# Kernel optimization log

Hardware: AMD Instinct MI355X
Metric: run time of the kernel (lower is better)

Reference implementation:

```python
import jax, jax.numpy as jnp
import numpy as np

N = 50000
E = 400000
F_IN = 128
NUM_CLASSES = 16
# (heads, out_channels, concat) per GATConv layer
LAYERS = [(8, 32, True), (8, 16, True), (8, 8, True), (1, NUM_CLASSES, False)]
DIMS_IN = [F_IN, 256, 128, 64]
NEG_SLOPE = 0.2
BN_EPS = 1e-5


def setup_inputs() -> dict:
    key = jax.random.key(0)
    ks = iter(jax.random.split(key, 64))
    inp = {}
    inp["x"] = jax.random.normal(next(ks), (N, F_IN), dtype=jnp.float32)
    inp["src"] = jax.random.randint(next(ks), (E,), 0, N, dtype=jnp.int32)
    inp["dst"] = jax.random.randint(next(ks), (E,), 0, N, dtype=jnp.int32)
    for l, ((h, c, concat), din) in enumerate(zip(LAYERS, DIMS_IN), start=1):
        s = 1.0 / np.sqrt(din)
        inp[f"W{l}"] = jax.random.normal(next(ks), (din, h * c), dtype=jnp.float32) * s
        inp[f"asrc{l}"] = jax.random.normal(next(ks), (h, c), dtype=jnp.float32) * 0.1
        inp[f"adst{l}"] = jax.random.normal(next(ks), (h, c), dtype=jnp.float32) * 0.1
        dout = h * c if concat else c
        inp[f"b{l}"] = jax.random.normal(next(ks), (dout,), dtype=jnp.float32) * 0.01
        inp[f"g{l}"] = jax.random.uniform(next(ks), (dout,), dtype=jnp.float32, minval=0.5, maxval=1.5)
        inp[f"be{l}"] = jax.random.normal(next(ks), (dout,), dtype=jnp.float32) * 0.1
        inp[f"rm{l}"] = jax.random.normal(next(ks), (dout,), dtype=jnp.float32) * 0.1
        inp[f"rv{l}"] = jax.random.uniform(next(ks), (dout,), dtype=jnp.float32, minval=0.5, maxval=1.5)
    return inp


def _gat_conv(x, src, dst, W, a_src, a_dst, bias, heads, ch, concat):
    n = x.shape[0]
    h = (x @ W).reshape(n, heads, ch)                     # [N,H,C]
    e_s = jnp.einsum('nhc,hc->nh', h, a_src)              # [N,H]
    e_d = jnp.einsum('nhc,hc->nh', h, a_dst)
    alpha = jax.nn.leaky_relu(e_s[src] + e_d[dst], NEG_SLOPE)   # [E,H]
    amax = jax.ops.segment_max(alpha, dst, num_segments=n)
    ex = jnp.exp(alpha - amax[dst])
    den = jax.ops.segment_sum(ex, dst, num_segments=n)
    attn = ex / (den[dst] + 1e-16)                        # [E,H]
    out = jax.ops.segment_sum(h[src] * attn[:, :, None], dst, num_segments=n)  # [N,H,C]
    out = out.reshape(n, heads * ch) if concat else out.mean(axis=1)
    return out + bias


def _bn(x, g, b, rm, rv):
    return (x - rm) * jax.lax.rsqrt(rv + BN_EPS) * g + b


def _forward(x, src, dst, params):
    # PyG GATConv adds self-loops by default
    loops = jnp.arange(N, dtype=src.dtype)
    s = jnp.concatenate([src, loops])
    d = jnp.concatenate([dst, loops])
    out = x
    for l, (h, c, concat) in enumerate(LAYERS, start=1):
        W, a_s, a_d, b, g, be, rm, rv = (params[f"{k}{l}"] for k in
                                         ("W", "asrc", "adst", "b", "g", "be", "rm", "rv"))
        out = _gat_conv(out, s, d, W, a_s, a_d, b, h, c, concat)
        if l < 4:
            out = jax.nn.elu(out)
        out = _bn(out, g, be, rm, rv)
    return out


def reference(x, src, dst,
              W1, asrc1, adst1, b1, g1, be1, rm1, rv1,
              W2, asrc2, adst2, b2, g2, be2, rm2, rv2,
              W3, asrc3, adst3, b3, g3, be3, rm3, rv3,
              W4, asrc4, adst4, b4, g4, be4, rm4, rv4):
    params = dict(
        W1=W1, asrc1=asrc1, adst1=adst1, b1=b1, g1=g1, be1=be1, rm1=rm1, rv1=rv1,
        W2=W2, asrc2=asrc2, adst2=adst2, b2=b2, g2=g2, be2=be2, rm2=rm2, rv2=rv2,
        W3=W3, asrc3=asrc3, adst3=adst3, b3=b3, g3=g3, be3=be3, rm3=rm3, rv3=rv3,
        W4=W4, asrc4=asrc4, adst4=adst4, b4=b4, g4=g4, be4=be4, rm4=rm4, rv4=rv4)
    return _forward(x, src, dst, params)
```

## Files before the change

### kernel.cpp

```cpp
#include <hip/hip_runtime.h>

#define NEG_SLOPE 0.2f
#define BN_EPS 1e-5f

typedef unsigned short u16;
typedef unsigned int u32;
typedef __bf16 bf16x8 __attribute__((ext_vector_type(8)));
typedef float f32x4 __attribute__((ext_vector_type(4)));

__device__ __forceinline__ u32 f2bf(float f) {
    u32 u = __float_as_uint(f);
    return (u + 0x7FFFu + ((u >> 16) & 1u)) >> 16;
}
__device__ __forceinline__ float bf2f(u32 h) { return __uint_as_float(h << 16); }
__device__ __forceinline__ float bfl(u32 p) { return __uint_as_float(p << 16); }
__device__ __forceinline__ float bfh(u32 p) { return __uint_as_float(p & 0xFFFF0000u); }

__global__ void split_kernel(const float4* __restrict__ X, uint2* __restrict__ hi,
                             uint2* __restrict__ lo, int n4) {
    int i = blockIdx.x * blockDim.x + threadIdx.x;
    if (i >= n4) return;
    float4 v = X[i];
    u32 h0 = f2bf(v.x), h1 = f2bf(v.y), h2 = f2bf(v.z), h3 = f2bf(v.w);
    hi[i] = make_uint2(h0 | (h1 << 16), h2 | (h3 << 16));
    u32 l0 = f2bf(v.x - bf2f(h0)), l1 = f2bf(v.y - bf2f(h1)),
        l2 = f2bf(v.z - bf2f(h2)), l3 = f2bf(v.w - bf2f(h3));
    lo[i] = make_uint2(l0 | (l1 << 16), l2 | (l3 << 16));
}

__global__ void wt_prep(const float* __restrict__ W, u16* __restrict__ hi,
                        u16* __restrict__ lo, int K, int N) {
    int i = blockIdx.x * blockDim.x + threadIdx.x;
    if (i >= K * N) return;
    int k = i / N, n = i - k * N;
    float w = W[i];
    u32 h = f2bf(w);
    hi[n * K + k] = (u16)h;
    lo[n * K + k] = (u16)f2bf(w - bf2f(h));
}

template<int BN>
__launch_bounds__(256)
__global__ void gemm_mfma(const u16* __restrict__ Ahi, const u16* __restrict__ Alo,
                          const u16* __restrict__ Bhi, const u16* __restrict__ Blo,
                          u16* __restrict__ Cbf, int M, int K, int N) {
    constexpr int FM = (BN == 128) ? 4 : 2;
    __shared__ uint4 sA[2][512];
    __shared__ uint4 sB[2][BN * 4];
    const int tid = threadIdx.x;
    const int bm = blockIdx.y * 128;
    const int bn = blockIdx.x * BN;
    const int lane = tid & 63;
    const int w = tid >> 6;
    const int wm = (BN == 128) ? (w >> 1) * 64 : w * 32;
    const int wn = (BN == 128) ? (w & 1) * 64 : 0;
    const int fr = lane & 15;
    const int fs = lane >> 4;
    f32x4 zero = {0.f, 0.f, 0.f, 0.f};
    f32x4 acc[FM][4];
    #pragma unroll
    for (int i = 0; i < FM; i++)
        #pragma unroll
        for (int j = 0; j < 4; j++) acc[i][j] = zero;

    const int r0 = tid >> 2;
    const int ss = tid & 3;
    const int r1 = r0 + 64;
    const int d0 = r0 * 4 + (ss ^ ((r0 >> 1) & 3));
    const int d1 = r1 * 4 + (ss ^ ((r1 >> 1) & 3));

    for (int k0 = 0; k0 < K; k0 += 32) {
        {
            int gr = bm + r0;
            uint4 vh = make_uint4(0, 0, 0, 0), vl = make_uint4(0, 0, 0, 0);
            if (gr < M) {
                vh = *(const uint4*)(Ahi + (size_t)gr * K + k0 + ss * 8);
                vl = *(const uint4*)(Alo + (size_t)gr * K + k0 + ss * 8);
            }
            sA[0][d0] = vh; sA[1][d0] = vl;
            gr = bm + r1;
            vh = make_uint4(0, 0, 0, 0); vl = make_uint4(0, 0, 0, 0);
            if (gr < M) {
                vh = *(const uint4*)(Ahi + (size_t)gr * K + k0 + ss * 8);
                vl = *(const uint4*)(Alo + (size_t)gr * K + k0 + ss * 8);
            }
            sA[0][d1] = vh; sA[1][d1] = vl;
        }
        {
            int gr = bn + r0;
            sB[0][d0] = *(const uint4*)(Bhi + (size_t)gr * K + k0 + ss * 8);
            sB[1][d0] = *(const uint4*)(Blo + (size_t)gr * K + k0 + ss * 8);
            if constexpr (BN == 128) {
                gr = bn + r1;
                sB[0][d1] = *(const uint4*)(Bhi + (size_t)gr * K + k0 + ss * 8);
                sB[1][d1] = *(const uint4*)(Blo + (size_t)gr * K + k0 + ss * 8);
            }
        }
        __syncthreads();
        bf16x8 ah[FM], al[FM], bh[4], bl[4];
        #pragma unroll
        for (int mi = 0; mi < FM; mi++) {
            int row = wm + mi * 16 + fr;
            int idx = row * 4 + (fs ^ ((row >> 1) & 3));
            ah[mi] = *reinterpret_cast<const bf16x8*>(&sA[0][idx]);
            al[mi] = *reinterpret_cast<const bf16x8*>(&sA[1][idx]);
        }
        #pragma unroll
        for (int ni = 0; ni < 4; ni++) {
            int row = wn + ni * 16 + fr;
            int idx = row * 4 + (fs ^ ((row >> 1) & 3));
            bh[ni] = *reinterpret_cast<const bf16x8*>(&sB[0][idx]);
            bl[ni] = *reinterpret_cast<const bf16x8*>(&sB[1][idx]);
        }
        #pragma unroll
        for (int mi = 0; mi < FM; mi++)
            #pragma unroll
            for (int ni = 0; ni < 4; ni++) {
                acc[mi][ni] = __builtin_amdgcn_mfma_f32_16x16x32_bf16(ah[mi], bh[ni], acc[mi][ni], 0, 0, 0);
                acc[mi][ni] = __builtin_amdgcn_mfma_f32_16x16x32_bf16(ah[mi], bl[ni], acc[mi][ni], 0, 0, 0);
                acc[mi][ni] = __builtin_amdgcn_mfma_f32_16x16x32_bf16(al[mi], bh[ni], acc[mi][ni], 0, 0, 0);
            }
        __syncthreads();
    }
    #pragma unroll
    for (int mi = 0; mi < FM; mi++) {
        #pragma unroll
        for (int ni = 0; ni < 4; ni++) {
            int colg = bn + wn + ni * 16 + fr;
            int rbase = bm + wm + mi * 16 + fs * 4;
            #pragma unroll
            for (int r = 0; r < 4; r++) {
                int rw = rbase + r;
                if (rw < M) Cbf[(size_t)rw * N + colg] = (u16)f2bf(acc[mi][ni][r]);
            }
        }
    }
}

__launch_bounds__(256)
__global__ void gemm_k64n16(const float* __restrict__ A, const float* __restrict__ B,
                            u16* __restrict__ Cbf, int M) {
    __shared__ float As[64][68];
    __shared__ float Bs[64][16];
    const int tid = threadIdx.x;
    const int bm = blockIdx.x * 64;
    {
        int r = tid >> 2, c = (tid & 3) << 2;
        *reinterpret_cast<float4*>(&Bs[r][c]) = *reinterpret_cast<const float4*>(&B[r * 16 + c]);
    }
    #pragma unroll
    for (int p = 0; p < 4; p++) {
        int m = (tid >> 4) + p * 16;
        int c = (tid & 15) << 2;
        int gm = bm + m;
        float4 v = make_float4(0.f, 0.f, 0.f, 0.f);
        if (gm < M) v = *reinterpret_cast<const float4*>(&A[(size_t)gm * 64 + c]);
        *reinterpret_cast<float4*>(&As[m][c]) = v;
    }
    __syncthreads();
    const int tc = tid & 15;
    const int r0 = tid >> 4;
    float acc[4] = {};
    #pragma unroll
    for (int k4 = 0; k4 < 16; k4++) {
        float b0 = Bs[4 * k4 + 0][tc];
        float b1 = Bs[4 * k4 + 1][tc];
        float b2 = Bs[4 * k4 + 2][tc];
        float b3 = Bs[4 * k4 + 3][tc];
        #pragma unroll
        for (int i = 0; i < 4; i++) {
            float4 av = *reinterpret_cast<const float4*>(&As[r0 + i * 16][4 * k4]);
            acc[i] += av.x * b0 + av.y * b1 + av.z * b2 + av.w * b3;
        }
    }
    #pragma unroll
    for (int i = 0; i < 4; i++) {
        int m = bm + r0 + i * 16;
        if (m < M) Cbf[(size_t)m * 16 + tc] = (u16)f2bf(acc[i]);
    }
}

__global__ void scores_kernel(const u16* __restrict__ h,
                              const float* __restrict__ asrc,
                              const float* __restrict__ adst,
                              float* __restrict__ es, float* __restrict__ ed,
                              int Nn, int H, int C) {
    int idx = blockIdx.x * blockDim.x + threadIdx.x;
    if (idx >= Nn * H) return;
    int n = idx / H, hh = idx % H;
    const u16* hp = h + ((size_t)n * H + hh) * C;
    const float4* ap = reinterpret_cast<const float4*>(asrc + hh * C);
    const float4* bp = reinterpret_cast<const float4*>(adst + hh * C);
    float s = 0.f, d = 0.f;
    for (int c4 = 0; c4 < C / 4; c4++) {
        uint2 pv = *reinterpret_cast<const uint2*>(hp + 4 * c4);
        float v0 = bfl(pv.x), v1 = bfh(pv.x), v2 = bfl(pv.y), v3 = bfh(pv.y);
        float4 a = ap[c4], b = bp[c4];
        s += v0 * a.x + v1 * a.y + v2 * a.z + v3 * a.w;
        d += v0 * b.x + v1 * b.y + v2 * b.z + v3 * b.w;
    }
    es[idx] = s;
    ed[idx] = d;
}

__global__ void hist_kernel(const int* __restrict__ dst, int* __restrict__ counts,
                            int E0, int Etot) {
    int e = blockIdx.x * blockDim.x + threadIdx.x;
    if (e >= Etot) return;
    int d_ = (e < E0) ? dst[e] : e - E0;
    atomicAdd(&counts[d_], 1);
}

__global__ void scan_kernel(const int* __restrict__ counts, int* __restrict__ row_ptr, int Nn) {
    __shared__ int wsum[16];
    __shared__ int chunk_total;
    __shared__ int carry_s;
    const int tid = threadIdx.x;
    const int lane = tid & 63;
    const int wid = tid >> 6;
    if (tid == 0) carry_s = 0;
    __syncthreads();
    for (int base = 0; base < Nn; base += 1024) {
        int i = base + tid;
        int v = (i < Nn) ? counts[i] : 0;
        int iv = v;
        #pragma unroll
        for (int off = 1; off < 64; off <<= 1) {
            int t = __shfl_up(iv, off, 64);
            if (lane >= off) iv += t;
        }
        if (lane == 63) wsum[wid] = iv;
        __syncthreads();
        if (tid == 0) {
            int s = 0;
            #pragma unroll
            for (int k = 0; k < 16; k++) { int t = wsum[k]; wsum[k] = s; s += t; }
            chunk_total = s;
        }
        __syncthreads();
        if (i < Nn) row_ptr[i] = carry_s + wsum[wid] + (iv - v);
        __syncthreads();
        if (tid == 0) carry_s += chunk_total;
        __syncthreads();
    }
    if (tid == 0) row_ptr[Nn] = carry_s;
}

__global__ void scatter_kernel(const int* __restrict__ src, const int* __restrict__ dst,
                               int* __restrict__ cursor, int* __restrict__ col,
                               int E0, int Etot) {
    int e = blockIdx.x * blockDim.x + threadIdx.x;
    if (e >= Etot) return;
    int d_ = (e < E0) ? dst[e] : e - E0;
    int s_ = (e < E0) ? src[e] : e - E0;
    int pos = atomicAdd(&cursor[d_], 1);
    col[pos] = s_;
}

template<int H, int C, int NT, int DO_ELU, int OUT_HILO>
__launch_bounds__(256)
__global__ void gat_fused(const int* __restrict__ row_ptr, const int* __restrict__ col,
                          const float* __restrict__ es, const float* __restrict__ ed,
                          const u16* __restrict__ h16, float* __restrict__ outf,
                          u16* __restrict__ outh, u16* __restrict__ outl,
                          const float* __restrict__ bias, const float* __restrict__ g,
                          const float* __restrict__ be, const float* __restrict__ rm,
                          const float* __restrict__ rv, int Nn) {
    constexpr int Dout = H * C;
    constexpr int VEC = Dout / NT;
    constexpr int NPB = 256 / NT;
    constexpr int CH = 32;
    __shared__ float w_s[NPB][CH][H];
    __shared__ int   c_s[NPB][CH];
    const int tid = threadIdx.x;
    const int slot = tid / NT;
    const int t = tid % NT;
    const int node = blockIdx.x * NPB + slot;
    if (node >= Nn) return;
    const int jb = row_ptr[node], je = row_ptr[node + 1];
    float edv[H];
    if constexpr (H == 8) {
        float4 e0 = *reinterpret_cast<const float4*>(&ed[node * 8]);
        float4 e1 = *reinterpret_cast<const float4*>(&ed[node * 8 + 4]);
        edv[0] = e0.x; edv[1] = e0.y; edv[2] = e0.z; edv[3] = e0.w;
        edv[4] = e1.x; edv[5] = e1.y; edv[6] = e1.z; edv[7] = e1.w;
    } else {
        edv[0] = ed[node];
    }
    const int c0 = t * VEC;
    const int hh = c0 / C;
    float acc[VEC] = {};
    float den = 0.f;
    for (int j0 = jb; j0 < je; j0 += CH) {
        int cnt = je - j0;
        if (cnt > CH) cnt = CH;
        for (int tt = t; tt < cnt; tt += NT) {
            int s = col[j0 + tt];
            c_s[slot][tt] = s;
            if constexpr (H == 8) {
                float4 q0 = *reinterpret_cast<const float4*>(&es[s * 8]);
                float4 q1 = *reinterpret_cast<const float4*>(&es[s * 8 + 4]);
                float al8[8] = {q0.x, q0.y, q0.z, q0.w, q1.x, q1.y, q1.z, q1.w};
                #pragma unroll
                for (int h2 = 0; h2 < 8; h2++) {
                    float a = al8[h2] + edv[h2];
                    a = (a >= 0.f) ? a : NEG_SLOPE * a;
                    w_s[slot][tt][h2] = __expf(a);
                }
            } else {
                float a = es[s] + edv[0];
                a = (a >= 0.f) ? a : NEG_SLOPE * a;
                w_s[slot][tt][0] = __expf(a);
            }
        }
        asm volatile("s_waitcnt lgkmcnt(0)" ::: "memory");
        int j = 0;
        for (; j + 4 <= cnt; j += 4) {
            int sx[4]; float ww[4];
            #pragma unroll
            for (int u = 0; u < 4; u++) { sx[u] = c_s[slot][j + u]; ww[u] = w_s[slot][j + u][hh]; }
            if constexpr (VEC == 8) {
                uint4 pv[4];
                #pragma unroll
                for (int u = 0; u < 4; u++)
                    pv[u] = *reinterpret_cast<const uint4*>(h16 + (size_t)sx[u] * Dout + c0);
                #pragma unroll
                for (int u = 0; u < 4; u++) {
                    den += ww[u];
                    acc[0] += ww[u] * bfl(pv[u].x); acc[1] += ww[u] * bfh(pv[u].x);
                    acc[2] += ww[u] * bfl(pv[u].y); acc[3] += ww[u] * bfh(pv[u].y);
                    acc[4] += ww[u] * bfl(pv[u].z); acc[5] += ww[u] * bfh(pv[u].z);
                    acc[6] += ww[u] * bfl(pv[u].w); acc[7] += ww[u] * bfh(pv[u].w);
                }
            } else {
                uint2 pv[4];
                #pragma unroll
                for (int u = 0; u < 4; u++)
                    pv[u] = *reinterpret_cast<const uint2*>(h16 + (size_t)sx[u] * Dout + c0);
                #pragma unroll
                for (int u = 0; u < 4; u++) {
                    den += ww[u];
                    acc[0] += ww[u] * bfl(pv[u].x); acc[1] += ww[u] * bfh(pv[u].x);
                    acc[2] += ww[u] * bfl(pv[u].y); acc[3] += ww[u] * bfh(pv[u].y);
                }
            }
        }
        for (; j < cnt; j++) {
            float w = w_s[slot][j][hh];
            den += w;
            const u16* hp = h16 + (size_t)c_s[slot][j] * Dout + c0;
            if constexpr (VEC == 8) {
                uint4 pv = *reinterpret_cast<const uint4*>(hp);
                acc[0] += w * bfl(pv.x); acc[1] += w * bfh(pv.x);
                acc[2] += w * bfl(pv.y); acc[3] += w * bfh(pv.y);
                acc[4] += w * bfl(pv.z); acc[5] += w * bfh(pv.z);
                acc[6] += w * bfl(pv.w); acc[7] += w * bfh(pv.w);
            } else {
                uint2 pv = *reinterpret_cast<const uint2*>(hp);
                acc[0] += w * bfl(pv.x); acc[1] += w * bfh(pv.x);
                acc[2] += w * bfl(pv.y); acc[3] += w * bfh(pv.y);
            }
        }
        asm volatile("s_waitcnt lgkmcnt(0)" ::: "memory");
    }
    const float inv = 1.f / (den + 1e-16f);
    float res[VEC];
    #pragma unroll
    for (int v = 0; v < VEC; v++) {
        const int jc = c0 + v;
        float y = acc[v] * inv + bias[jc];
        if (DO_ELU) y = (y > 0.f) ? y : expm1f(y);
        y = (y - rm[jc]) * rsqrtf(rv[jc] + BN_EPS) * g[jc] + be[jc];
        res[v] = y;
    }
    if constexpr (OUT_HILO) {
        u32 rh[VEC], rl[VEC];
        #pragma unroll
        for (int v = 0; v < VEC; v++) {
            rh[v] = f2bf(res[v]);
            rl[v] = f2bf(res[v] - bf2f(rh[v]));
        }
        if constexpr (VEC == 8) {
            uint4 ph = make_uint4(rh[0] | (rh[1] << 16), rh[2] | (rh[3] << 16),
                                  rh[4] | (rh[5] << 16), rh[6] | (rh[7] << 16));
            uint4 pl = make_uint4(rl[0] | (rl[1] << 16), rl[2] | (rl[3] << 16),
                                  rl[4] | (rl[5] << 16), rl[6] | (rl[7] << 16));
            *reinterpret_cast<uint4*>(outh + (size_t)node * Dout + c0) = ph;
            *reinterpret_cast<uint4*>(outl + (size_t)node * Dout + c0) = pl;
        } else {
            uint2 ph = make_uint2(rh[0] | (rh[1] << 16), rh[2] | (rh[3] << 16));
            uint2 pl = make_uint2(rl[0] | (rl[1] << 16), rl[2] | (rl[3] << 16));
            *reinterpret_cast<uint2*>(outh + (size_t)node * Dout + c0) = ph;
            *reinterpret_cast<uint2*>(outl + (size_t)node * Dout + c0) = pl;
        }
    } else {
        float* op = outf + (size_t)node * Dout + c0;
        if constexpr (VEC == 8) {
            *reinterpret_cast<float4*>(op) = make_float4(res[0], res[1], res[2], res[3]);
            *reinterpret_cast<float4*>(op + 4) = make_float4(res[4], res[5], res[6], res[7]);
        } else {
            *reinterpret_cast<float4*>(op) = make_float4(res[0], res[1], res[2], res[3]);
        }
    }
}

extern "C" void kernel_launch(void* const* d_in, const int* in_sizes, int n_in,
                              void* d_out, int out_size, void* d_ws, size_t ws_size,
                              hipStream_t stream) {
    const float* x = (const float*)d_in[0];
    const int* src = (const int*)d_in[1];
    const int* dst = (const int*)d_in[2];
    const int Nn = in_sizes[0] / 128;
    const int E0 = in_sizes[1];
    const int Etot = E0 + Nn;

    u16* A0 = (u16*)d_ws;
    u16* Bh = A0 + (size_t)Nn * 512;
    u16* Ch = Bh + (size_t)Nn * 256;
    float* es = (float*)(Ch + (size_t)Nn * 256);
    float* ed = es + (size_t)Nn * 8;
    int* row_ptr = (int*)(ed + (size_t)Nn * 8);
    int* cursor  = row_ptr + (Nn + 1);
    int* col     = cursor + Nn;
    u16* wth = (u16*)(col + Etot);
    u16* wtl = wth + 65536;

    u16* XH = A0;
    u16* XL = A0 + (size_t)Nn * 128;
    u16* Y1H = A0;
    u16* Y1L = A0 + (size_t)Nn * 256;
    u16* Y2H = Ch;
    u16* Y2L = Ch + (size_t)Nn * 128;
    float* out3 = (float*)A0;

    hipMemsetAsync(cursor, 0, sizeof(int) * Nn, stream);
    hist_kernel<<<(Etot + 255) / 256, 256, 0, stream>>>(dst, cursor, E0, Etot);
    scan_kernel<<<1, 1024, 0, stream>>>(cursor, row_ptr, Nn);
    hipMemcpyAsync(cursor, row_ptr, sizeof(int) * Nn, hipMemcpyDeviceToDevice, stream);
    scatter_kernel<<<(Etot + 255) / 256, 256, 0, stream>>>(src, dst, cursor, col, E0, Etot);

    const int gy128 = (Nn + 127) / 128;

    for (int l = 0; l < 4; l++) {
        const float* const* p = (const float* const*)(d_in + 3 + l * 8);
        const float* W    = p[0];
        const float* asrc = p[1];
        const float* adst = p[2];
        const float* bias = p[3];
        const float* g    = p[4];
        const float* be   = p[5];
        const float* rm   = p[6];
        const float* rv   = p[7];

        if (l == 0) {
            const int K = 128, N = 256;
            int n4 = Nn * K / 4;
            split_kernel<<<(n4 + 255) / 256, 256, 0, stream>>>(
                (const float4*)x, (uint2*)XH, (uint2*)XL, n4);
            wt_prep<<<(K * N + 255) / 256, 256, 0, stream>>>(W, wth, wtl, K, N);
            gemm_mfma<128><<<dim3(N / 128, gy128), 256, 0, stream>>>(XH, XL, wth, wtl, Bh, Nn, K, N);
            scores_kernel<<<(Nn * 8 + 255) / 256, 256, 0, stream>>>(Bh, asrc, adst, es, ed, Nn, 8, 32);
            gat_fused<8, 32, 32, 1, 1><<<(Nn + 7) / 8, 256, 0, stream>>>(
                row_ptr, col, es, ed, Bh, nullptr, Y1H, Y1L, bias, g, be, rm, rv, Nn);
        } else if (l == 1) {
            const int K = 256, N = 128;
            wt_prep<<<(K * N + 255) / 256, 256, 0, stream>>>(W, wth, wtl, K, N);
            gemm_mfma<128><<<dim3(1, gy128), 256, 0, stream>>>(Y1H, Y1L, wth, wtl, Bh, Nn, K, N);
            scores_kernel<<<(Nn * 8 + 255) / 256, 256, 0, stream>>>(Bh, asrc, adst, es, ed, Nn, 8, 16);
            gat_fused<8, 16, 16, 1, 1><<<(Nn + 15) / 16, 256, 0, stream>>>(
                row_ptr, col, es, ed, Bh, nullptr, Y2H, Y2L, bias, g, be, rm, rv, Nn);
        } else if (l == 2) {
            const int K = 128, N = 64;
            wt_prep<<<(K * N + 255) / 256, 256, 0, stream>>>(W, wth, wtl, K, N);
            gemm_mfma<64><<<dim3(1, gy128), 256, 0, stream>>>(Y2H, Y2L, wth, wtl, Bh, Nn, K, N);
            scores_kernel<<<(Nn * 8 + 255) / 256, 256, 0, stream>>>(Bh, asrc, adst, es, ed, Nn, 8, 8);
            gat_fused<8, 8, 16, 1, 0><<<(Nn + 15) / 16, 256, 0, stream>>>(
                row_ptr, col, es, ed, Bh, out3, nullptr, nullptr, bias, g, be, rm, rv, Nn);
        } else {
            gemm_k64n16<<<(Nn + 63) / 64, 256, 0, stream>>>(out3, W, Bh, Nn);
            scores_kernel<<<(Nn + 255) / 256, 256, 0, stream>>>(Bh, asrc, adst, es, ed, Nn, 1, 16);
            gat_fused<1, 16, 4, 0, 0><<<(Nn + 63) / 64, 256, 0, stream>>>(
                row_ptr, col, es, ed, Bh, (float*)d_out, nullptr, nullptr, bias, g, be, rm, rv, Nn);
        }
    }
}
```

Baseline: 458.6 us.

## Store features head-major and split GAT aggregation across heads via grid y

The GEMM epilogue now writes projected features in a head-major [H][N][C] layout, and the score kernel writes es/ed head-major as well. The fused aggregation kernel is rewritten so each block handles one head (blockIdx.y) and each thread owns 4 channels. It recomputes the attention weight per edge directly instead of staging weights and indices in shared memory. The intent is to shrink each head's gather working set for cache locality and to drop the LDS staging. The cost is that col, row_ptr and the exp computation are repeated once per head, and the GEMM stores become more scattered.

```diff
diff --git a/kernel.cpp b/kernel.cpp
--- a/kernel.cpp
+++ b/kernel.cpp
@@ -39,7 +39,7 @@
     lo[n * K + k] = (u16)f2bf(w - bf2f(h));
 }
 
-template<int BN>
+template<int BN, int HMC>
 __launch_bounds__(256)
 __global__ void gemm_mfma(const u16* __restrict__ Ahi, const u16* __restrict__ Alo,
                           const u16* __restrict__ Bhi, const u16* __restrict__ Blo,
@@ -131,7 +131,14 @@
             #pragma unroll
             for (int r = 0; r < 4; r++) {
                 int rw = rbase + r;
-                if (rw < M) Cbf[(size_t)rw * N + colg] = (u16)f2bf(acc[mi][ni][r]);
+                if (rw >= M) continue;
+                u16 val = (u16)f2bf(acc[mi][ni][r]);
+                if constexpr (HMC > 0) {
+                    int hh2 = colg / HMC, cc2 = colg - hh2 * HMC;
+                    Cbf[((size_t)hh2 * M + rw) * HMC + cc2] = val;
+                } else {
+                    Cbf[(size_t)rw * N + colg] = val;
+                }
             }
         }
     }
@@ -188,7 +195,7 @@
     int idx = blockIdx.x * blockDim.x + threadIdx.x;
     if (idx >= Nn * H) return;
     int n = idx / H, hh = idx % H;
-    const u16* hp = h + ((size_t)n * H + hh) * C;
+    const u16* hp = h + ((size_t)hh * Nn + n) * C;
     const float4* ap = reinterpret_cast<const float4*>(asrc + hh * C);
     const float4* bp = reinterpret_cast<const float4*>(adst + hh * C);
     float s = 0.f, d = 0.f;
@@ -199,8 +206,8 @@
         s += v0 * a.x + v1 * a.y + v2 * a.z + v3 * a.w;
         d += v0 * b.x + v1 * b.y + v2 * b.z + v3 * b.w;
     }
-    es[idx] = s;
-    ed[idx] = d;
+    es[(size_t)hh * Nn + n] = s;
+    ed[(size_t)hh * Nn + n] = d;
 }
 
 __global__ void hist_kernel(const int* __restrict__ dst, int* __restrict__ counts,
@@ -267,140 +274,70 @@
                           const float* __restrict__ be, const float* __restrict__ rm,
                           const float* __restrict__ rv, int Nn) {
     constexpr int Dout = H * C;
-    constexpr int VEC = Dout / NT;
     constexpr int NPB = 256 / NT;
-    constexpr int CH = 32;
-    __shared__ float w_s[NPB][CH][H];
-    __shared__ int   c_s[NPB][CH];
     const int tid = threadIdx.x;
-    const int slot = tid / NT;
+    const int node = blockIdx.x * NPB + tid / NT;
     const int t = tid % NT;
-    const int node = blockIdx.x * NPB + slot;
+    const int hh = blockIdx.y;
     if (node >= Nn) return;
     const int jb = row_ptr[node], je = row_ptr[node + 1];
-    float edv[H];
-    if constexpr (H == 8) {
-        float4 e0 = *reinterpret_cast<const float4*>(&ed[node * 8]);
-        float4 e1 = *reinterpret_cast<const float4*>(&ed[node * 8 + 4]);
-        edv[0] = e0.x; edv[1] = e0.y; edv[2] = e0.z; edv[3] = e0.w;
-        edv[4] = e1.x; edv[5] = e1.y; edv[6] = e1.z; edv[7] = e1.w;
-    } else {
-        edv[0] = ed[node];
-    }
-    const int c0 = t * VEC;
-    const int hh = c0 / C;
-    float acc[VEC] = {};
-    float den = 0.f;
-    for (int j0 = jb; j0 < je; j0 += CH) {
-        int cnt = je - j0;
-        if (cnt > CH) cnt = CH;
-        for (int tt = t; tt < cnt; tt += NT) {
-            int s = col[j0 + tt];
-            c_s[slot][tt] = s;
-            if constexpr (H == 8) {
-                float4 q0 = *reinterpret_cast<const float4*>(&es[s * 8]);
-                float4 q1 = *reinterpret_cast<const float4*>(&es[s * 8 + 4]);
-                float al8[8] = {q0.x, q0.y, q0.z, q0.w, q1.x, q1.y, q1.z, q1.w};
-                #pragma unroll
-                for (int h2 = 0; h2 < 8; h2++) {
-                    float a = al8[h2] + edv[h2];
-                    a = (a >= 0.f) ? a : NEG_SLOPE * a;
-                    w_s[slot][tt][h2] = __expf(a);
-                }
-            } else {
-                float a = es[s] + edv[0];
-                a = (a >= 0.f) ? a : NEG_SLOPE * a;
-                w_s[slot][tt][0] = __expf(a);
-            }
-        }
-        asm volatile("s_waitcnt lgkmcnt(0)" ::: "memory");
-        int j = 0;
-        for (; j + 4 <= cnt; j += 4) {
-            int sx[4]; float ww[4];
-            #pragma unroll
-            for (int u = 0; u < 4; u++) { sx[u] = c_s[slot][j + u]; ww[u] = w_s[slot][j + u][hh]; }
-            if constexpr (VEC == 8) {
-                uint4 pv[4];
-                #pragma unroll
-                for (int u = 0; u < 4; u++)
-                    pv[u] = *reinterpret_cast<const uint4*>(h16 + (size_t)sx[u] * Dout + c0);
-                #pragma unroll
-                for (int u = 0; u < 4; u++) {
-                    den += ww[u];
-                    acc[0] += ww[u] * bfl(pv[u].x); acc[1] += ww[u] * bfh(pv[u].x);
-                    acc[2] += ww[u] * bfl(pv[u].y); acc[3] += ww[u] * bfh(pv[u].y);
-                    acc[4] += ww[u] * bfl(pv[u].z); acc[5] += ww[u] * bfh(pv[u].z);
-                    acc[6] += ww[u] * bfl(pv[u].w); acc[7] += ww[u] * bfh(pv[u].w);
-                }
-            } else {
-                uint2 pv[4];
-                #pragma unroll
-                for (int u = 0; u < 4; u++)
-                    pv[u] = *reinterpret_cast<const uint2*>(h16 + (size_t)sx[u] * Dout + c0);
-                #pragma unroll
-                for (int u = 0; u < 4; u++) {
-                    den += ww[u];
-                    acc[0] += ww[u] * bfl(pv[u].x); acc[1] += ww[u] * bfh(pv[u].x);
-                    acc[2] += ww[u] * bfl(pv[u].y); acc[3] += ww[u] * bfh(pv[u].y);
-                }
-            }
-        }
-        for (; j < cnt; j++) {
-            float w = w_s[slot][j][hh];
-            den += w;
-            const u16* hp = h16 + (size_t)c_s[slot][j] * Dout + c0;
-            if constexpr (VEC == 8) {
-                uint4 pv = *reinterpret_cast<const uint4*>(hp);
-                acc[0] += w * bfl(pv.x); acc[1] += w * bfh(pv.x);
-                acc[2] += w * bfl(pv.y); acc[3] += w * bfh(pv.y);
-                acc[4] += w * bfl(pv.z); acc[5] += w * bfh(pv.z);
-                acc[6] += w * bfl(pv.w); acc[7] += w * bfh(pv.w);
-            } else {
-                uint2 pv = *reinterpret_cast<const uint2*>(hp);
-                acc[0] += w * bfl(pv.x); acc[1] += w * bfh(pv.x);
-                acc[2] += w * bfl(pv.y); acc[3] += w * bfh(pv.y);
-            }
-        }
-        asm volatile("s_waitcnt lgkmcnt(0)" ::: "memory");
+    const float* esh = es + (size_t)hh * Nn;
+    const float edv = ed[(size_t)hh * Nn + node];
+    const u16* hb = h16 + (size_t)hh * Nn * C + t * 4;
+    float a0c = 0.f, a1c = 0.f, a2c = 0.f, a3c = 0.f, den = 0.f;
+    int j = jb;
+    for (; j + 4 <= je; j += 4) {
+        int s0 = col[j], s1 = col[j + 1], s2 = col[j + 2], s3 = col[j + 3];
+        float e0 = esh[s0] + edv, e1 = esh[s1] + edv, e2 = esh[s2] + edv, e3 = esh[s3] + edv;
+        uint2 p0 = *reinterpret_cast<const uint2*>(hb + (size_t)s0 * C);
+        uint2 p1 = *reinterpret_cast<const uint2*>(hb + (size_t)s1 * C);
+        uint2 p2 = *reinterpret_cast<const uint2*>(hb + (size_t)s2 * C);
+        uint2 p3 = *reinterpret_cast<const uint2*>(hb + (size_t)s3 * C);
+        e0 = (e0 >= 0.f) ? e0 : NEG_SLOPE * e0;
+        e1 = (e1 >= 0.f) ? e1 : NEG_SLOPE * e1;
+        e2 = (e2 >= 0.f) ? e2 : NEG_SLOPE * e2;
+        e3 = (e3 >= 0.f) ? e3 : NEG_SLOPE * e3;
+        float w0 = __expf(e0), w1 = __expf(e1), w2 = __expf(e2), w3 = __expf(e3);
+        den += (w0 + w1) + (w2 + w3);
+        a0c += w0 * bfl(p0.x) + w1 * bfl(p1.x) + w2 * bfl(p2.x) + w3 * bfl(p3.x);
+        a1c += w0 * bfh(p0.x) + w1 * bfh(p1.x) + w2 * bfh(p2.x) + w3 * bfh(p3.x);
+        a2c += w0 * bfl(p0.y) + w1 * bfl(p1.y) + w2 * bfl(p2.y) + w3 * bfl(p3.y);
+        a3c += w0 * bfh(p0.y) + w1 * bfh(p1.y) + w2 * bfh(p2.y) + w3 * bfh(p3.y);
+    }
+    for (; j < je; j++) {
+        int s = col[j];
+        float a = esh[s] + edv;
+        a = (a >= 0.f) ? a : NEG_SLOPE * a;
+        float w = __expf(a);
+        uint2 pv = *reinterpret_cast<const uint2*>(hb + (size_t)s * C);
+        den += w;
+        a0c += w * bfl(pv.x); a1c += w * bfh(pv.x);
+        a2c += w * bfl(pv.y); a3c += w * bfh(pv.y);
     }
     const float inv = 1.f / (den + 1e-16f);
-    float res[VEC];
-    #pragma unroll
-    for (int v = 0; v < VEC; v++) {
-        const int jc = c0 + v;
-        float y = acc[v] * inv + bias[jc];
+    const int jc = hh * C + t * 4;
+    float res[4] = {a0c, a1c, a2c, a3c};
+    #pragma unroll
+    for (int v = 0; v < 4; v++) {
+        float y = res[v] * inv + bias[jc + v];
         if (DO_ELU) y = (y > 0.f) ? y : expm1f(y);
-        y = (y - rm[jc]) * rsqrtf(rv[jc] + BN_EPS) * g[jc] + be[jc];
+        y = (y - rm[jc + v]) * rsqrtf(rv[jc + v] + BN_EPS) * g[jc + v] + be[jc + v];
         res[v] = y;
     }
     if constexpr (OUT_HILO) {
-        u32 rh[VEC], rl[VEC];
-        #pragma unroll
-        for (int v = 0; v < VEC; v++) {
+        u32 rh[4], rl[4];
+        #pragma unroll
+        for (int v = 0; v < 4; v++) {
             rh[v] = f2bf(res[v]);
             rl[v] = f2bf(res[v] - bf2f(rh[v]));
         }
-        if constexpr (VEC == 8) {
-            uint4 ph = make_uint4(rh[0] | (rh[1] << 16), rh[2] | (rh[3] << 16),
-                                  rh[4] | (rh[5] << 16), rh[6] | (rh[7] << 16));
-            uint4 pl = make_uint4(rl[0] | (rl[1] << 16), rl[2] | (rl[3] << 16),
-                                  rl[4] | (rl[5] << 16), rl[6] | (rl[7] << 16));
-            *reinterpret_cast<uint4*>(outh + (size_t)node * Dout + c0) = ph;
-            *reinterpret_cast<uint4*>(outl + (size_t)node * Dout + c0) = pl;
-        } else {
-            uint2 ph = make_uint2(rh[0] | (rh[1] << 16), rh[2] | (rh[3] << 16));
-            uint2 pl = make_uint2(rl[0] | (rl[1] << 16), rl[2] | (rl[3] << 16));
-            *reinterpret_cast<uint2*>(outh + (size_t)node * Dout + c0) = ph;
-            *reinterpret_cast<uint2*>(outl + (size_t)node * Dout + c0) = pl;
-        }
+        uint2 ph = make_uint2(rh[0] | (rh[1] << 16), rh[2] | (rh[3] << 16));
+        uint2 pl = make_uint2(rl[0] | (rl[1] << 16), rl[2] | (rl[3] << 16));
+        *reinterpret_cast<uint2*>(outh + (size_t)node * Dout + jc) = ph;
+        *reinterpret_cast<uint2*>(outl + (size_t)node * Dout + jc) = pl;
     } else {
-        float* op = outf + (size_t)node * Dout + c0;
-        if constexpr (VEC == 8) {
-            *reinterpret_cast<float4*>(op) = make_float4(res[0], res[1], res[2], res[3]);
-            *reinterpret_cast<float4*>(op + 4) = make_float4(res[4], res[5], res[6], res[7]);
-        } else {
-            *reinterpret_cast<float4*>(op) = make_float4(res[0], res[1], res[2], res[3]);
-        }
+        *reinterpret_cast<float4*>(outf + (size_t)node * Dout + jc) =
+            make_float4(res[0], res[1], res[2], res[3]);
     }
 }
 
@@ -458,28 +395,28 @@
             split_kernel<<<(n4 + 255) / 256, 256, 0, stream>>>(
                 (const float4*)x, (uint2*)XH, (uint2*)XL, n4);
             wt_prep<<<(K * N + 255) / 256, 256, 0, stream>>>(W, wth, wtl, K, N);
-            gemm_mfma<128><<<dim3(N / 128, gy128), 256, 0, stream>>>(XH, XL, wth, wtl, Bh, Nn, K, N);
+            gemm_mfma<128, 32><<<dim3(N / 128, gy128), 256, 0, stream>>>(XH, XL, wth, wtl, Bh, Nn, K, N);
             scores_kernel<<<(Nn * 8 + 255) / 256, 256, 0, stream>>>(Bh, asrc, adst, es, ed, Nn, 8, 32);
-            gat_fused<8, 32, 32, 1, 1><<<(Nn + 7) / 8, 256, 0, stream>>>(
+            gat_fused<8, 32, 8, 1, 1><<<dim3((Nn + 31) / 32, 8), 256, 0, stream>>>(
                 row_ptr, col, es, ed, Bh, nullptr, Y1H, Y1L, bias, g, be, rm, rv, Nn);
         } else if (l == 1) {
             const int K = 256, N = 128;
             wt_prep<<<(K * N + 255) / 256, 256, 0, stream>>>(W, wth, wtl, K, N);
-            gemm_mfma<128><<<dim3(1, gy128), 256, 0, stream>>>(Y1H, Y1L, wth, wtl, Bh, Nn, K, N);
+            gemm_mfma<128, 16><<<dim3(1, gy128), 256, 0, stream>>>(Y1H, Y1L, wth, wtl, Bh, Nn, K, N);
             scores_kernel<<<(Nn * 8 + 255) / 256, 256, 0, stream>>>(Bh, asrc, adst, es, ed, Nn, 8, 16);
-            gat_fused<8, 16, 16, 1, 1><<<(Nn + 15) / 16, 256, 0, stream>>>(
+            gat_fused<8, 16, 4, 1, 1><<<dim3((Nn + 63) / 64, 8), 256, 0, stream>>>(
                 row_ptr, col, es, ed, Bh, nullptr, Y2H, Y2L, bias, g, be, rm, rv, Nn);
         } else if (l == 2) {
             const int K = 128, N = 64;
             wt_prep<<<(K * N + 255) / 256, 256, 0, stream>>>(W, wth, wtl, K, N);
-            gemm_mfma<64><<<dim3(1, gy128), 256, 0, stream>>>(Y2H, Y2L, wth, wtl, Bh, Nn, K, N);
+            gemm_mfma<64, 8><<<dim3(1, gy128), 256, 0, stream>>>(Y2H, Y2L, wth, wtl, Bh, Nn, K, N);
             scores_kernel<<<(Nn * 8 + 255) / 256, 256, 0, stream>>>(Bh, asrc, adst, es, ed, Nn, 8, 8);
-            gat_fused<8, 8, 16, 1, 0><<<(Nn + 15) / 16, 256, 0, stream>>>(
+            gat_fused<8, 8, 2, 1, 0><<<dim3((Nn + 127) / 128, 8), 256, 0, stream>>>(
                 row_ptr, col, es, ed, Bh, out3, nullptr, nullptr, bias, g, be, rm, rv, Nn);
         } else {
             gemm_k64n16<<<(Nn + 63) / 64, 256, 0, stream>>>(out3, W, Bh, Nn);
             scores_kernel<<<(Nn + 255) / 256, 256, 0, stream>>>(Bh, asrc, adst, es, ed, Nn, 1, 16);
-            gat_fused<1, 16, 4, 0, 0><<<(Nn + 63) / 64, 256, 0, stream>>>(
+            gat_fused<1, 16, 4, 0, 0><<<dim3((Nn + 63) / 64, 1), 256, 0, stream>>>(
                 row_ptr, col, es, ed, Bh, (float*)d_out, nullptr, nullptr, bias, g, be, rm, rv, Nn);
         }
     }
```

New measurement: 405.3 us. -11.6%, faster.
